# Kernel tuning notes

Hardware: AMD Instinct MI355X
Metric: run time of the kernel (lower is better)

## Reference

```python
import jax, jax.numpy as jnp
import numpy as np

N_NODES = 50000
N_EDGES = 800000
IN_CH, HID_CH, OUT_CH = 256, 128, 64


def setup_inputs() -> dict:
    key = jax.random.key(0)
    k_x, k_e, k_w1, k_w2 = jax.random.split(key, 4)
    x = jax.random.normal(k_x, (N_NODES, IN_CH), dtype=jnp.float32)
    edge_index = jax.random.randint(k_e, (2, N_EDGES), 0, N_NODES, dtype=jnp.int32)
    # Glorot-style init like PyG GCNConv (weight [in, out], bias zeros)
    s1 = float(np.sqrt(6.0 / (IN_CH + HID_CH)))
    s2 = float(np.sqrt(6.0 / (HID_CH + OUT_CH)))
    W1 = jax.random.uniform(k_w1, (IN_CH, HID_CH), jnp.float32, -s1, s1)
    b1 = jnp.zeros((HID_CH,), jnp.float32)
    W2 = jax.random.uniform(k_w2, (HID_CH, OUT_CH), jnp.float32, -s2, s2)
    b2 = jnp.zeros((OUT_CH,), jnp.float32)
    return {"x": x, "edge_index": edge_index, "W1": W1, "b1": b1, "W2": W2, "b2": b2}


def _gcn_conv(x, src, dst, deg_inv_sqrt, W, b, n_nodes):
    """GCNConv with self-loops: D^{-1/2}(A+I)D^{-1/2} X W + b."""
    h = x @ W  # [N, out]
    norm = deg_inv_sqrt[src] * deg_inv_sqrt[dst]          # [E]
    msgs = h[src] * norm[:, None]                          # [E, out] gather
    agg = jax.ops.segment_sum(msgs, dst, num_segments=n_nodes)  # scatter-add
    self_loop = h * (deg_inv_sqrt * deg_inv_sqrt)[:, None]      # self-loop term
    return agg + self_loop + b


def reference(x, edge_index, W1, b1, W2, b2):
    n = x.shape[0]
    src, dst = edge_index[0], edge_index[1]
    # degree includes self-loop (+1), edge weight 1, counted at destination
    deg = jnp.zeros((n,), x.dtype).at[dst].add(1.0) + 1.0
    dis = jax.lax.rsqrt(deg)
    h = jax.nn.relu(_gcn_conv(x, src, dst, dis, W1, b1, n))
    out = jax.nn.relu(_gcn_conv(h, src, dst, dis, W2, b2, n))
    return out
```

## Files before the change

### kernel.cpp

```cpp
#include <hip/hip_runtime.h>

#define N_NODES 50000
#define N_EDGES 800000
#define IN_CH 256
#define HID_CH 128
#define OUT_CH 64
#define CAP 64
#define NBINS 196
#define PCHUNK 3200
#define PBLOCKS 250
#define SWZ_ELEMS (IN_CH * HID_CH + HID_CH * OUT_CH)
#define SWZ_BLOCKS (SWZ_ELEMS / 256)

typedef _Float16 f16;
typedef _Float16 f16x8 __attribute__((ext_vector_type(8)));
typedef float f32x4 __attribute__((ext_vector_type(4)));
typedef unsigned short u16;
typedef unsigned int u32;

template <int K, int N>
__device__ __forceinline__ void swz(const float* __restrict__ W, f16* __restrict__ Bsw,
                                    int idx) {
    constexpr int NTILES = N / 16;
    int j = idx & 7;
    int lane = (idx >> 3) & 63;
    int rest = idx >> 9;
    int nt = rest % NTILES;
    int ks = rest / NTILES;
    int k = ks * 32 + (lane >> 4) * 8 + j;
    int n = nt * 16 + (lane & 15);
    Bsw[idx] = (f16)W[(size_t)k * N + n];
}

__device__ __forceinline__ void scan_local(const int* __restrict__ binCnt,
                                           int* sc, int* vv) {
    const int t = threadIdx.x;
    int v = (t < NBINS) ? binCnt[t] : 0;
    sc[t] = v; vv[t] = v;
    __syncthreads();
    for (int ofs = 1; ofs < 256; ofs <<= 1) {
        int add = (t >= ofs) ? sc[t - ofs] : 0;
        __syncthreads();
        sc[t] += add;
        __syncthreads();
    }
}

__global__ __launch_bounds__(256) void k_pre(const int* __restrict__ dst,
                                             int* __restrict__ binCnt,
                                             const float* __restrict__ W1,
                                             const float* __restrict__ W2,
                                             f16* __restrict__ B1,
                                             f16* __restrict__ B2) {
    if ((int)blockIdx.x < PBLOCKS) {
        __shared__ int lcnt[NBINS];
        for (int i = threadIdx.x; i < NBINS; i += 256) lcnt[i] = 0;
        __syncthreads();
        int base = blockIdx.x * PCHUNK;
        for (int i = base + (int)threadIdx.x; i < base + PCHUNK; i += 256)
            atomicAdd(&lcnt[dst[i] >> 8], 1);
        __syncthreads();
        for (int i = threadIdx.x; i < NBINS; i += 256)
            if (lcnt[i]) atomicAdd(&binCnt[i], lcnt[i]);
        return;
    }
    int idx = ((int)blockIdx.x - PBLOCKS) * 256 + threadIdx.x;
    if (idx < IN_CH * HID_CH) {
        swz<IN_CH, HID_CH>(W1, B1, idx);
    } else {
        idx -= IN_CH * HID_CH;
        if (idx < HID_CH * OUT_CH) swz<HID_CH, OUT_CH>(W2, B2, idx);
    }
}

__global__ __launch_bounds__(256) void k_place(const int* __restrict__ src,
                                               const int* __restrict__ dst,
                                               const int* __restrict__ binCnt,
                                               int* __restrict__ binCursor,
                                               u32* __restrict__ ebuf, int E) {
    __shared__ u32 codes[PCHUNK];
    __shared__ int sc[256], vv[256];
    __shared__ int lcnt[NBINS], lbase[NBINS], lcur[NBINS];
    scan_local(binCnt, sc, vv);
    for (int i = threadIdx.x; i < NBINS; i += 256) lcnt[i] = 0;
    __syncthreads();
    int base = blockIdx.x * PCHUNK;
    int m = min(PCHUNK, E - base);
    for (int j = threadIdx.x; j < m; j += 256) {
        u32 d = (u32)dst[base + j];
        codes[j] = (d << 16) | (u32)src[base + j];
        atomicAdd(&lcnt[d >> 8], 1);
    }
    __syncthreads();
    for (int i = threadIdx.x; i < NBINS; i += 256) {
        lbase[i] = (sc[i] - vv[i]) + atomicAdd(&binCursor[i], lcnt[i]);
        lcur[i] = 0;
    }
    __syncthreads();
    for (int j = threadIdx.x; j < m; j += 256) {
        u32 c = codes[j];
        int b = c >> 24;
        int p = atomicAdd(&lcur[b], 1);
        ebuf[lbase[b] + p] = c;
    }
}

__global__ __launch_bounds__(256) void k_build(const u32* __restrict__ ebuf,
                                               const int* __restrict__ binCnt,
                                               int* __restrict__ cnt,
                                               float* __restrict__ dis,
                                               u16* __restrict__ bucket, int N) {
    __shared__ int sc[256], vv[256];
    __shared__ int lcnt[256];
    __shared__ u16 lbuck[256 * CAP];
    scan_local(binCnt, sc, vv);
    int t = threadIdx.x;
    lcnt[t] = 0;
    __syncthreads();
    int b = blockIdx.x;
    int s = sc[b] - vv[b];
    int e = sc[b];
    for (int i = s + t; i < e; i += 256) {
        u32 c = ebuf[i];
        int local = (c >> 16) & 255;
        int p = atomicAdd(&lcnt[local], 1);
        if (p < CAP) lbuck[local * CAP + p] = (u16)(c & 0xFFFFu);
    }
    __syncthreads();
    int nodeBase = b << 8;
    if (nodeBase + t < N) {
        cnt[nodeBase + t] = lcnt[t];
        dis[nodeBase + t] = rsqrtf((float)lcnt[t] + 1.0f);
    }
    const uint4* lsrc = (const uint4*)lbuck;
    uint4* gdst = (uint4*)(bucket + (size_t)nodeBase * CAP);
    for (int idx = t; idx < 256 * CAP / 8; idx += 256) {
        int row = idx >> 3;
        int chunk = idx & 7;
        if (nodeBase + row < N && (chunk << 3) < lcnt[row]) gdst[idx] = lsrc[idx];
    }
}

template <int K, int N, bool A_FP32, bool RELU>
__global__ __launch_bounds__(256) void k_gemm(const void* __restrict__ Av,
                                              const f16* __restrict__ Bsw,
                                              const float* __restrict__ dis,
                                              f16* __restrict__ C, int M) {
    constexpr int KSTEPS = K / 32, NTILES = N / 16;
    const int tid = threadIdx.x;
    const int wave = tid >> 6, lane = tid & 63;
    const int quad = lane >> 4, l16 = lane & 15;
    int row = blockIdx.x * 64 + wave * 16 + l16;
    const int rowc = row < M ? row : M - 1;

    f32x4 acc[NTILES];
#pragma unroll
    for (int t = 0; t < NTILES; ++t) acc[t] = (f32x4){0.f, 0.f, 0.f, 0.f};

#pragma unroll
    for (int ks = 0; ks < KSTEPS; ++ks) {
        f16x8 afrag;
        if (A_FP32) {
            const float* A = (const float*)Av;
            const float4* p = (const float4*)(A + (size_t)rowc * K + ks * 32 + quad * 8);
            float4 v0 = p[0], v1 = p[1];
            afrag[0] = (f16)v0.x; afrag[1] = (f16)v0.y;
            afrag[2] = (f16)v0.z; afrag[3] = (f16)v0.w;
            afrag[4] = (f16)v1.x; afrag[5] = (f16)v1.y;
            afrag[6] = (f16)v1.z; afrag[7] = (f16)v1.w;
        } else {
            const f16* A = (const f16*)Av;
            afrag = *(const f16x8*)(A + (size_t)rowc * K + ks * 32 + quad * 8);
            if (RELU) {
#pragma unroll
                for (int j = 0; j < 8; ++j)
                    afrag[j] = afrag[j] > (f16)0 ? afrag[j] : (f16)0;
            }
        }
#pragma unroll
        for (int t = 0; t < NTILES; ++t) {
            f16x8 bfrag = *(const f16x8*)(Bsw + (((size_t)ks * NTILES + t) * 64 + lane) * 8);
            acc[t] = __builtin_amdgcn_mfma_f32_16x16x32_f16(afrag, bfrag, acc[t], 0, 0, 0);
        }
    }

    int rbase = blockIdx.x * 64 + wave * 16 + quad * 4;
#pragma unroll
    for (int r = 0; r < 4; ++r) {
        int gr = rbase + r;
        if (gr < M) {
            float d = dis[gr];
#pragma unroll
            for (int t = 0; t < NTILES; ++t)
                C[(size_t)gr * N + t * 16 + l16] = (f16)(acc[t][r] * d);
        }
    }
}

__global__ __launch_bounds__(256) void k_pullgemm(const f16* __restrict__ g1,
                                                  const float* __restrict__ dis,
                                                  const float* __restrict__ b1,
                                                  const int* __restrict__ cnt,
                                                  const u16* __restrict__ bucket,
                                                  const f16* __restrict__ B2sw,
                                                  f16* __restrict__ g2) {
    constexpr int LDSW = HID_CH + 8;
    __shared__ f16 aggl[64 * LDSW];
    const int tid = threadIdx.x;
    const int sub = tid & 15;
    const int nl = tid >> 4;
    const int blockBase = (int)blockIdx.x * 64;

    const float4* b1p = (const float4*)(b1 + sub * 8);
    float4 bb0 = b1p[0], bb1 = b1p[1];
    float bv[8] = {bb0.x, bb0.y, bb0.z, bb0.w, bb1.x, bb1.y, bb1.z, bb1.w};

    for (int it = 0; it < 4; ++it) {
        int lrow = it * 16 + nl;
        int u = blockBase + lrow;
        f16x8 o;
        if (u < N_NODES) {
            const f16* gp = g1 + sub * 8;
            f16x8 sv = *(const f16x8*)(gp + (size_t)u * HID_CH);
            float a[8];
#pragma unroll
            for (int j = 0; j < 8; ++j) a[j] = (float)sv[j];

            int n = cnt[u];
            if (n > CAP) n = CAP;
            const u16* row = bucket + u * CAP;

            int k = 0;
            for (; k + 8 <= n; k += 8) {
                uint4 iv = *(const uint4*)(row + k);
                int s0 = iv.x & 0xFFFF, s1 = iv.x >> 16;
                int s2 = iv.y & 0xFFFF, s3 = iv.y >> 16;
                int s4 = iv.z & 0xFFFF, s5 = iv.z >> 16;
                int s6 = iv.w & 0xFFFF, s7 = iv.w >> 16;
                f16x8 v0 = *(const f16x8*)(gp + (size_t)s0 * HID_CH);
                f16x8 v1 = *(const f16x8*)(gp + (size_t)s1 * HID_CH);
                f16x8 v2 = *(const f16x8*)(gp + (size_t)s2 * HID_CH);
                f16x8 v3 = *(const f16x8*)(gp + (size_t)s3 * HID_CH);
                f16x8 v4 = *(const f16x8*)(gp + (size_t)s4 * HID_CH);
                f16x8 v5 = *(const f16x8*)(gp + (size_t)s5 * HID_CH);
                f16x8 v6 = *(const f16x8*)(gp + (size_t)s6 * HID_CH);
                f16x8 v7 = *(const f16x8*)(gp + (size_t)s7 * HID_CH);
#pragma unroll
                for (int j = 0; j < 8; ++j)
                    a[j] += (((float)v0[j] + (float)v1[j]) + ((float)v2[j] + (float)v3[j])) +
                            (((float)v4[j] + (float)v5[j]) + ((float)v6[j] + (float)v7[j]));
            }
            if (k + 4 <= n) {
                ushort4 s4v = *(const ushort4*)(row + k);
                f16x8 v0 = *(const f16x8*)(gp + (size_t)s4v.x * HID_CH);
                f16x8 v1 = *(const f16x8*)(gp + (size_t)s4v.y * HID_CH);
                f16x8 v2 = *(const f16x8*)(gp + (size_t)s4v.z * HID_CH);
                f16x8 v3 = *(const f16x8*)(gp + (size_t)s4v.w * HID_CH);
#pragma unroll
                for (int j = 0; j < 8; ++j)
                    a[j] += ((float)v0[j] + (float)v1[j]) + ((float)v2[j] + (float)v3[j]);
                k += 4;
            }
            for (; k < n; ++k) {
                f16x8 v = *(const f16x8*)(gp + (size_t)row[k] * HID_CH);
#pragma unroll
                for (int j = 0; j < 8; ++j) a[j] += (float)v[j];
            }

            float du = dis[u];
#pragma unroll
            for (int j = 0; j < 8; ++j) {
                float t = fmaf(du, a[j], bv[j]);
                o[j] = (f16)(t > 0.f ? t : 0.f);
            }
        } else {
#pragma unroll
            for (int j = 0; j < 8; ++j) o[j] = (f16)0;
        }
        *(f16x8*)(aggl + (size_t)lrow * LDSW + sub * 8) = o;
    }
    __syncthreads();

    constexpr int KSTEPS = HID_CH / 32, NTILES = OUT_CH / 16;
    const int wave = tid >> 6, lane = tid & 63;
    const int quad = lane >> 4, l16 = lane & 15;
    const int lrowA = wave * 16 + l16;

    f32x4 acc[NTILES];
#pragma unroll
    for (int t = 0; t < NTILES; ++t) acc[t] = (f32x4){0.f, 0.f, 0.f, 0.f};

#pragma unroll
    for (int ks = 0; ks < KSTEPS; ++ks) {
        f16x8 afrag = *(const f16x8*)(aggl + (size_t)lrowA * LDSW + ks * 32 + quad * 8);
#pragma unroll
        for (int t = 0; t < NTILES; ++t) {
            f16x8 bfrag = *(const f16x8*)(B2sw + (((size_t)ks * NTILES + t) * 64 + lane) * 8);
            acc[t] = __builtin_amdgcn_mfma_f32_16x16x32_f16(afrag, bfrag, acc[t], 0, 0, 0);
        }
    }

    int rbase = blockBase + wave * 16 + quad * 4;
#pragma unroll
    for (int r = 0; r < 4; ++r) {
        int gr = rbase + r;
        if (gr < N_NODES) {
            float d = dis[gr];
#pragma unroll
            for (int t = 0; t < NTILES; ++t)
                g2[(size_t)gr * OUT_CH + t * 16 + l16] = (f16)(acc[t][r] * d);
        }
    }
}

__global__ __launch_bounds__(256) void k_pull2(const f16* __restrict__ g2,
                                               const float* __restrict__ dis,
                                               const float* __restrict__ b2,
                                               const int* __restrict__ cnt,
                                               const u16* __restrict__ bucket,
                                               float* __restrict__ out) {
    int gtid = blockIdx.x * 256 + threadIdx.x;
    int u = gtid >> 3;
    int sub = gtid & 7;
    if (u >= N_NODES) return;
    const f16* gp = g2 + sub * 8;

    f16x8 sv = *(const f16x8*)(gp + (size_t)u * OUT_CH);
    float a[8];
#pragma unroll
    for (int j = 0; j < 8; ++j) a[j] = (float)sv[j];

    int n = cnt[u];
    if (n > CAP) n = CAP;
    const u16* row = bucket + u * CAP;

    int k = 0;
    for (; k + 8 <= n; k += 8) {
        uint4 iv = *(const uint4*)(row + k);
        int s0 = iv.x & 0xFFFF, s1 = iv.x >> 16;
        int s2 = iv.y & 0xFFFF, s3 = iv.y >> 16;
        int s4 = iv.z & 0xFFFF, s5 = iv.z >> 16;
        int s6 = iv.w & 0xFFFF, s7 = iv.w >> 16;
        f16x8 v0 = *(const f16x8*)(gp + (size_t)s0 * OUT_CH);
        f16x8 v1 = *(const f16x8*)(gp + (size_t)s1 * OUT_CH);
        f16x8 v2 = *(const f16x8*)(gp + (size_t)s2 * OUT_CH);
        f16x8 v3 = *(const f16x8*)(gp + (size_t)s3 * OUT_CH);
        f16x8 v4 = *(const f16x8*)(gp + (size_t)s4 * OUT_CH);
        f16x8 v5 = *(const f16x8*)(gp + (size_t)s5 * OUT_CH);
        f16x8 v6 = *(const f16x8*)(gp + (size_t)s6 * OUT_CH);
        f16x8 v7 = *(const f16x8*)(gp + (size_t)s7 * OUT_CH);
#pragma unroll
        for (int j = 0; j < 8; ++j)
            a[j] += (((float)v0[j] + (float)v1[j]) + ((float)v2[j] + (float)v3[j])) +
                    (((float)v4[j] + (float)v5[j]) + ((float)v6[j] + (float)v7[j]));
    }
    if (k + 4 <= n) {
        ushort4 s4v = *(const ushort4*)(row + k);
        f16x8 v0 = *(const f16x8*)(gp + (size_t)s4v.x * OUT_CH);
        f16x8 v1 = *(const f16x8*)(gp + (size_t)s4v.y * OUT_CH);
        f16x8 v2 = *(const f16x8*)(gp + (size_t)s4v.z * OUT_CH);
        f16x8 v3 = *(const f16x8*)(gp + (size_t)s4v.w * OUT_CH);
#pragma unroll
        for (int j = 0; j < 8; ++j)
            a[j] += ((float)v0[j] + (float)v1[j]) + ((float)v2[j] + (float)v3[j]);
        k += 4;
    }
    for (; k < n; ++k) {
        f16x8 v = *(const f16x8*)(gp + (size_t)row[k] * OUT_CH);
#pragma unroll
        for (int j = 0; j < 8; ++j) a[j] += (float)v[j];
    }

    float du = dis[u];
    float4* op = (float4*)(out + (size_t)u * OUT_CH + sub * 8);
    float4 o0, o1;
    o0.x = fmaxf(fmaf(du, a[0], b2[sub * 8 + 0]), 0.f);
    o0.y = fmaxf(fmaf(du, a[1], b2[sub * 8 + 1]), 0.f);
    o0.z = fmaxf(fmaf(du, a[2], b2[sub * 8 + 2]), 0.f);
    o0.w = fmaxf(fmaf(du, a[3], b2[sub * 8 + 3]), 0.f);
    o1.x = fmaxf(fmaf(du, a[4], b2[sub * 8 + 4]), 0.f);
    o1.y = fmaxf(fmaf(du, a[5], b2[sub * 8 + 5]), 0.f);
    o1.z = fmaxf(fmaf(du, a[6], b2[sub * 8 + 6]), 0.f);
    o1.w = fmaxf(fmaf(du, a[7], b2[sub * 8 + 7]), 0.f);
    op[0] = o0;
    op[1] = o1;
}


extern "C" void kernel_launch(void* const* d_in, const int* in_sizes, int n_in,
                              void* d_out, int out_size, void* d_ws, size_t ws_size,
                              hipStream_t stream) {
    const float* x  = (const float*)d_in[0];
    const int* ei   = (const int*)d_in[1];
    const float* W1 = (const float*)d_in[2];
    const float* b1 = (const float*)d_in[3];
    const float* W2 = (const float*)d_in[4];
    const float* b2 = (const float*)d_in[5];
    float* out = (float*)d_out;

    const int* src = ei;
    const int* dst = ei + N_EDGES;

    char* ws = (char*)d_ws;
    size_t off = 0;
    auto alloc = [&](size_t bytes) -> void* {
        off = (off + 255) & ~(size_t)255;
        void* p = ws + off;
        off += bytes;
        return p;
    };
    int*   zbuf      = (int*)alloc((size_t)(NBINS * 2) * 4);
    int*   binCnt    = zbuf;
    int*   binCursor = zbuf + NBINS;
    u32*   ebuf      = (u32*)alloc((size_t)N_EDGES * 4);
    int*   cnt       = (int*)alloc((size_t)N_NODES * 4);
    float* dis       = (float*)alloc((size_t)N_NODES * 4);
    u16*   bucket    = (u16*)alloc((size_t)N_NODES * CAP * 2);
    f16*   W1sw      = (f16*)alloc((size_t)IN_CH * HID_CH * 2);
    f16*   W2sw      = (f16*)alloc((size_t)HID_CH * OUT_CH * 2);
    f16*   g1        = (f16*)alloc((size_t)N_NODES * HID_CH * 2);
    f16*   g2        = (f16*)alloc((size_t)N_NODES * OUT_CH * 2);

    hipMemsetAsync(zbuf, 0, (size_t)(NBINS * 2) * 4, stream);

    k_pre<<<PBLOCKS + SWZ_BLOCKS, 256, 0, stream>>>(dst, binCnt, W1, W2, W1sw, W2sw);
    k_place<<<PBLOCKS, 256, 0, stream>>>(src, dst, binCnt, binCursor, ebuf, N_EDGES);
    k_build<<<NBINS, 256, 0, stream>>>(ebuf, binCnt, cnt, dis, bucket, N_NODES);

    k_gemm<IN_CH, HID_CH, true, false><<<(N_NODES + 63) / 64, 256, 0, stream>>>(
        x, W1sw, dis, g1, N_NODES);

    k_pullgemm<<<(N_NODES + 63) / 64, 256, 0, stream>>>(g1, dis, b1, cnt, bucket,
                                                        W2sw, g2);

    k_pull2<<<(N_NODES * 8 + 255) / 256, 256, 0, stream>>>(g2, dis, b2, cnt, bucket, out);
}
```

Before: 198.5 us.

## Replace binned two-pass edge placement with direct global-atomic bucket scatter

Removes the three-kernel counting-sort pipeline (bin count, bin placement into an edge buffer, per-bin LDS bucket build) and replaces it with one kernel where each edge does a global atomicAdd on its destination's count and writes its source into a fixed-capacity per-node bucket. The degree normalisation is now computed inside the first GEMM's epilogue from cnt, so the separate dis write pass goes away. This saves two launches and the intermediate edge buffer traffic, but trades coalesced LDS-staged writes for 800K scattered global atomics and 2-byte scattered stores. Neighbour order within a bucket becomes nondeterministic, which can change floating-point summation order.

```diff
diff --git a/kernel.cpp b/kernel.cpp
--- a/kernel.cpp
+++ b/kernel.cpp
@@ -6,9 +6,7 @@
 #define HID_CH 128
 #define OUT_CH 64
 #define CAP 64
-#define NBINS 196
-#define PCHUNK 3200
-#define PBLOCKS 250
+#define SCAT_BLOCKS 3125
 #define SWZ_ELEMS (IN_CH * HID_CH + HID_CH * OUT_CH)
 #define SWZ_BLOCKS (SWZ_ELEMS / 256)
 
@@ -32,39 +30,23 @@
     Bsw[idx] = (f16)W[(size_t)k * N + n];
 }
 
-__device__ __forceinline__ void scan_local(const int* __restrict__ binCnt,
-                                           int* sc, int* vv) {
-    const int t = threadIdx.x;
-    int v = (t < NBINS) ? binCnt[t] : 0;
-    sc[t] = v; vv[t] = v;
-    __syncthreads();
-    for (int ofs = 1; ofs < 256; ofs <<= 1) {
-        int add = (t >= ofs) ? sc[t - ofs] : 0;
-        __syncthreads();
-        sc[t] += add;
-        __syncthreads();
-    }
-}
-
-__global__ __launch_bounds__(256) void k_pre(const int* __restrict__ dst,
-                                             int* __restrict__ binCnt,
-                                             const float* __restrict__ W1,
-                                             const float* __restrict__ W2,
-                                             f16* __restrict__ B1,
-                                             f16* __restrict__ B2) {
-    if ((int)blockIdx.x < PBLOCKS) {
-        __shared__ int lcnt[NBINS];
-        for (int i = threadIdx.x; i < NBINS; i += 256) lcnt[i] = 0;
-        __syncthreads();
-        int base = blockIdx.x * PCHUNK;
-        for (int i = base + (int)threadIdx.x; i < base + PCHUNK; i += 256)
-            atomicAdd(&lcnt[dst[i] >> 8], 1);
-        __syncthreads();
-        for (int i = threadIdx.x; i < NBINS; i += 256)
-            if (lcnt[i]) atomicAdd(&binCnt[i], lcnt[i]);
+__global__ __launch_bounds__(256) void k_scatter(const int* __restrict__ src,
+                                                 const int* __restrict__ dst,
+                                                 int* __restrict__ cnt,
+                                                 u16* __restrict__ bucket,
+                                                 const float* __restrict__ W1,
+                                                 const float* __restrict__ W2,
+                                                 f16* __restrict__ B1,
+                                                 f16* __restrict__ B2) {
+    if ((int)blockIdx.x < SCAT_BLOCKS) {
+        int i = (int)blockIdx.x * 256 + (int)threadIdx.x;
+        int d = dst[i];
+        int s = src[i];
+        int p = atomicAdd(&cnt[d], 1);
+        if (p < CAP) bucket[(size_t)d * CAP + p] = (u16)s;
         return;
     }
-    int idx = ((int)blockIdx.x - PBLOCKS) * 256 + threadIdx.x;
+    int idx = ((int)blockIdx.x - SCAT_BLOCKS) * 256 + threadIdx.x;
     if (idx < IN_CH * HID_CH) {
         swz<IN_CH, HID_CH>(W1, B1, idx);
     } else {
@@ -73,79 +55,12 @@
     }
 }
 
-__global__ __launch_bounds__(256) void k_place(const int* __restrict__ src,
-                                               const int* __restrict__ dst,
-                                               const int* __restrict__ binCnt,
-                                               int* __restrict__ binCursor,
-                                               u32* __restrict__ ebuf, int E) {
-    __shared__ u32 codes[PCHUNK];
-    __shared__ int sc[256], vv[256];
-    __shared__ int lcnt[NBINS], lbase[NBINS], lcur[NBINS];
-    scan_local(binCnt, sc, vv);
-    for (int i = threadIdx.x; i < NBINS; i += 256) lcnt[i] = 0;
-    __syncthreads();
-    int base = blockIdx.x * PCHUNK;
-    int m = min(PCHUNK, E - base);
-    for (int j = threadIdx.x; j < m; j += 256) {
-        u32 d = (u32)dst[base + j];
-        codes[j] = (d << 16) | (u32)src[base + j];
-        atomicAdd(&lcnt[d >> 8], 1);
-    }
-    __syncthreads();
-    for (int i = threadIdx.x; i < NBINS; i += 256) {
-        lbase[i] = (sc[i] - vv[i]) + atomicAdd(&binCursor[i], lcnt[i]);
-        lcur[i] = 0;
-    }
-    __syncthreads();
-    for (int j = threadIdx.x; j < m; j += 256) {
-        u32 c = codes[j];
-        int b = c >> 24;
-        int p = atomicAdd(&lcur[b], 1);
-        ebuf[lbase[b] + p] = c;
-    }
-}
-
-__global__ __launch_bounds__(256) void k_build(const u32* __restrict__ ebuf,
-                                               const int* __restrict__ binCnt,
-                                               int* __restrict__ cnt,
+template <int K, int N>
+__global__ __launch_bounds__(256) void k_gemm1(const float* __restrict__ A,
+                                               const f16* __restrict__ Bsw,
+                                               const int* __restrict__ cnt,
                                                float* __restrict__ dis,
-                                               u16* __restrict__ bucket, int N) {
-    __shared__ int sc[256], vv[256];
-    __shared__ int lcnt[256];
-    __shared__ u16 lbuck[256 * CAP];
-    scan_local(binCnt, sc, vv);
-    int t = threadIdx.x;
-    lcnt[t] = 0;
-    __syncthreads();
-    int b = blockIdx.x;
-    int s = sc[b] - vv[b];
-    int e = sc[b];
-    for (int i = s + t; i < e; i += 256) {
-        u32 c = ebuf[i];
-        int local = (c >> 16) & 255;
-        int p = atomicAdd(&lcnt[local], 1);
-        if (p < CAP) lbuck[local * CAP + p] = (u16)(c & 0xFFFFu);
-    }
-    __syncthreads();
-    int nodeBase = b << 8;
-    if (nodeBase + t < N) {
-        cnt[nodeBase + t] = lcnt[t];
-        dis[nodeBase + t] = rsqrtf((float)lcnt[t] + 1.0f);
-    }
-    const uint4* lsrc = (const uint4*)lbuck;
-    uint4* gdst = (uint4*)(bucket + (size_t)nodeBase * CAP);
-    for (int idx = t; idx < 256 * CAP / 8; idx += 256) {
-        int row = idx >> 3;
-        int chunk = idx & 7;
-        if (nodeBase + row < N && (chunk << 3) < lcnt[row]) gdst[idx] = lsrc[idx];
-    }
-}
-
-template <int K, int N, bool A_FP32, bool RELU>
-__global__ __launch_bounds__(256) void k_gemm(const void* __restrict__ Av,
-                                              const f16* __restrict__ Bsw,
-                                              const float* __restrict__ dis,
-                                              f16* __restrict__ C, int M) {
+                                               f16* __restrict__ C, int M) {
     constexpr int KSTEPS = K / 32, NTILES = N / 16;
     const int tid = threadIdx.x;
     const int wave = tid >> 6, lane = tid & 63;
@@ -160,23 +75,12 @@
 #pragma unroll
     for (int ks = 0; ks < KSTEPS; ++ks) {
         f16x8 afrag;
-        if (A_FP32) {
-            const float* A = (const float*)Av;
-            const float4* p = (const float4*)(A + (size_t)rowc * K + ks * 32 + quad * 8);
-            float4 v0 = p[0], v1 = p[1];
-            afrag[0] = (f16)v0.x; afrag[1] = (f16)v0.y;
-            afrag[2] = (f16)v0.z; afrag[3] = (f16)v0.w;
-            afrag[4] = (f16)v1.x; afrag[5] = (f16)v1.y;
-            afrag[6] = (f16)v1.z; afrag[7] = (f16)v1.w;
-        } else {
-            const f16* A = (const f16*)Av;
-            afrag = *(const f16x8*)(A + (size_t)rowc * K + ks * 32 + quad * 8);
-            if (RELU) {
-#pragma unroll
-                for (int j = 0; j < 8; ++j)
-                    afrag[j] = afrag[j] > (f16)0 ? afrag[j] : (f16)0;
-            }
-        }
+        const float4* p = (const float4*)(A + (size_t)rowc * K + ks * 32 + quad * 8);
+        float4 v0 = p[0], v1 = p[1];
+        afrag[0] = (f16)v0.x; afrag[1] = (f16)v0.y;
+        afrag[2] = (f16)v0.z; afrag[3] = (f16)v0.w;
+        afrag[4] = (f16)v1.x; afrag[5] = (f16)v1.y;
+        afrag[6] = (f16)v1.z; afrag[7] = (f16)v1.w;
 #pragma unroll
         for (int t = 0; t < NTILES; ++t) {
             f16x8 bfrag = *(const f16x8*)(Bsw + (((size_t)ks * NTILES + t) * 64 + lane) * 8);
@@ -189,7 +93,8 @@
     for (int r = 0; r < 4; ++r) {
         int gr = rbase + r;
         if (gr < M) {
-            float d = dis[gr];
+            float d = rsqrtf((float)cnt[gr] + 1.0f);
+            if (l16 == 0) dis[gr] = d;
 #pragma unroll
             for (int t = 0; t < NTILES; ++t)
                 C[(size_t)gr * N + t * 16 + l16] = (f16)(acc[t][r] * d);
@@ -409,10 +314,6 @@
         off += bytes;
         return p;
     };
-    int*   zbuf      = (int*)alloc((size_t)(NBINS * 2) * 4);
-    int*   binCnt    = zbuf;
-    int*   binCursor = zbuf + NBINS;
-    u32*   ebuf      = (u32*)alloc((size_t)N_EDGES * 4);
     int*   cnt       = (int*)alloc((size_t)N_NODES * 4);
     float* dis       = (float*)alloc((size_t)N_NODES * 4);
     u16*   bucket    = (u16*)alloc((size_t)N_NODES * CAP * 2);
@@ -421,14 +322,13 @@
     f16*   g1        = (f16*)alloc((size_t)N_NODES * HID_CH * 2);
     f16*   g2        = (f16*)alloc((size_t)N_NODES * OUT_CH * 2);
 
-    hipMemsetAsync(zbuf, 0, (size_t)(NBINS * 2) * 4, stream);
-
-    k_pre<<<PBLOCKS + SWZ_BLOCKS, 256, 0, stream>>>(dst, binCnt, W1, W2, W1sw, W2sw);
-    k_place<<<PBLOCKS, 256, 0, stream>>>(src, dst, binCnt, binCursor, ebuf, N_EDGES);
-    k_build<<<NBINS, 256, 0, stream>>>(ebuf, binCnt, cnt, dis, bucket, N_NODES);
-
-    k_gemm<IN_CH, HID_CH, true, false><<<(N_NODES + 63) / 64, 256, 0, stream>>>(
-        x, W1sw, dis, g1, N_NODES);
+    hipMemsetAsync(cnt, 0, (size_t)N_NODES * 4, stream);
+
+    k_scatter<<<SCAT_BLOCKS + SWZ_BLOCKS, 256, 0, stream>>>(src, dst, cnt, bucket,
+                                                            W1, W2, W1sw, W2sw);
+
+    k_gemm1<IN_CH, HID_CH><<<(N_NODES + 63) / 64, 256, 0, stream>>>(
+        x, W1sw, cnt, dis, g1, N_NODES);
 
     k_pullgemm<<<(N_NODES + 63) / 64, 256, 0, stream>>>(g1, dis, b1, cnt, bucket,
                                                         W2sw, g2);
```

Measured after the change: 206.4 us. +4.0%, slower.

## Store hidden features in column-tiled layout and stage neighbor lists in LDS

Applied to the files above, without the earlier changes.

The GEMM outputs g1 and g2 are now written in a tile-major layout, [tile][node][16], so each gather pass over one 16-column tile touches a compact 1.6 MB (g1) or smaller array that can stay in cache. The pull kernels first copy each block's neighbor index lists, counts and degree scales into shared memory, then loop over column tiles with 4 threads per node. This aims to improve L2 hit rate for the random gathers and to avoid re-reading indices from global memory. In exchange, indices are re-walked once per tile, each gather moves only 16 bytes, and the extra LDS use may lower occupancy.

```diff
diff --git a/kernel.cpp b/kernel.cpp
--- a/kernel.cpp
+++ b/kernel.cpp
@@ -6,11 +6,14 @@
 #define HID_CH 128
 #define OUT_CH 64
 #define CAP 64
+#define LBSTRIDE 72
 #define NBINS 196
 #define PCHUNK 3200
 #define PBLOCKS 250
 #define SWZ_ELEMS (IN_CH * HID_CH + HID_CH * OUT_CH)
 #define SWZ_BLOCKS (SWZ_ELEMS / 256)
+#define NT1 (HID_CH / 16)
+#define NT2 (OUT_CH / 16)
 
 typedef _Float16 f16;
 typedef _Float16 f16x8 __attribute__((ext_vector_type(8)));
@@ -141,11 +144,11 @@
     }
 }
 
-template <int K, int N, bool A_FP32, bool RELU>
-__global__ __launch_bounds__(256) void k_gemm(const void* __restrict__ Av,
-                                              const f16* __restrict__ Bsw,
-                                              const float* __restrict__ dis,
-                                              f16* __restrict__ C, int M) {
+__global__ __launch_bounds__(256) void k_gemm1(const float* __restrict__ A,
+                                               const f16* __restrict__ Bsw,
+                                               const float* __restrict__ dis,
+                                               f16* __restrict__ C, int M) {
+    constexpr int K = IN_CH, N = HID_CH;
     constexpr int KSTEPS = K / 32, NTILES = N / 16;
     const int tid = threadIdx.x;
     const int wave = tid >> 6, lane = tid & 63;
@@ -160,23 +163,12 @@
 #pragma unroll
     for (int ks = 0; ks < KSTEPS; ++ks) {
         f16x8 afrag;
-        if (A_FP32) {
-            const float* A = (const float*)Av;
-            const float4* p = (const float4*)(A + (size_t)rowc * K + ks * 32 + quad * 8);
-            float4 v0 = p[0], v1 = p[1];
-            afrag[0] = (f16)v0.x; afrag[1] = (f16)v0.y;
-            afrag[2] = (f16)v0.z; afrag[3] = (f16)v0.w;
-            afrag[4] = (f16)v1.x; afrag[5] = (f16)v1.y;
-            afrag[6] = (f16)v1.z; afrag[7] = (f16)v1.w;
-        } else {
-            const f16* A = (const f16*)Av;
-            afrag = *(const f16x8*)(A + (size_t)rowc * K + ks * 32 + quad * 8);
-            if (RELU) {
-#pragma unroll
-                for (int j = 0; j < 8; ++j)
-                    afrag[j] = afrag[j] > (f16)0 ? afrag[j] : (f16)0;
-            }
-        }
+        const float4* p = (const float4*)(A + (size_t)rowc * K + ks * 32 + quad * 8);
+        float4 v0 = p[0], v1 = p[1];
+        afrag[0] = (f16)v0.x; afrag[1] = (f16)v0.y;
+        afrag[2] = (f16)v0.z; afrag[3] = (f16)v0.w;
+        afrag[4] = (f16)v1.x; afrag[5] = (f16)v1.y;
+        afrag[6] = (f16)v1.z; afrag[7] = (f16)v1.w;
 #pragma unroll
         for (int t = 0; t < NTILES; ++t) {
             f16x8 bfrag = *(const f16x8*)(Bsw + (((size_t)ks * NTILES + t) * 64 + lane) * 8);
@@ -192,82 +184,102 @@
             float d = dis[gr];
 #pragma unroll
             for (int t = 0; t < NTILES; ++t)
-                C[(size_t)gr * N + t * 16 + l16] = (f16)(acc[t][r] * d);
-        }
-    }
-}
-
-__global__ __launch_bounds__(256) void k_pullgemm(const f16* __restrict__ g1,
+                C[((size_t)t * N_NODES + gr) * 16 + l16] = (f16)(acc[t][r] * d);
+        }
+    }
+}
+
+__global__ __launch_bounds__(256) void k_pullgemm(const f16* __restrict__ g1t,
                                                   const float* __restrict__ dis,
                                                   const float* __restrict__ b1,
                                                   const int* __restrict__ cnt,
                                                   const u16* __restrict__ bucket,
                                                   const f16* __restrict__ B2sw,
-                                                  f16* __restrict__ g2) {
+                                                  f16* __restrict__ g2t) {
     constexpr int LDSW = HID_CH + 8;
     __shared__ f16 aggl[64 * LDSW];
+    __shared__ u16 lbuck[64 * LBSTRIDE];
+    __shared__ int lcnt[64];
+    __shared__ float ldis[64];
     const int tid = threadIdx.x;
-    const int sub = tid & 15;
-    const int nl = tid >> 4;
     const int blockBase = (int)blockIdx.x * 64;
-
-    const float4* b1p = (const float4*)(b1 + sub * 8);
-    float4 bb0 = b1p[0], bb1 = b1p[1];
-    float bv[8] = {bb0.x, bb0.y, bb0.z, bb0.w, bb1.x, bb1.y, bb1.z, bb1.w};
-
-    for (int it = 0; it < 4; ++it) {
-        int lrow = it * 16 + nl;
-        int u = blockBase + lrow;
+    const int gmax = N_NODES - blockBase;
+
+    {
+        const uint4* bsrc = (const uint4*)(bucket + (size_t)blockBase * CAP);
+        for (int i = tid; i < 64 * (CAP / 8); i += 256) {
+            int r = i >> 3, c = i & 7;
+            uint4 v = make_uint4(0, 0, 0, 0);
+            if (r < gmax) v = bsrc[(r << 3) + c];
+            *(uint4*)(lbuck + r * LBSTRIDE + (c << 3)) = v;
+        }
+        if (tid < 64) {
+            int u = blockBase + tid;
+            int n = (u < N_NODES) ? cnt[u] : 0;
+            lcnt[tid] = n > CAP ? CAP : n;
+            ldis[tid] = (u < N_NODES) ? dis[u] : 0.f;
+        }
+    }
+    __syncthreads();
+
+    const int sub = tid & 1;
+    const int sl = (tid >> 1) & 1;
+    const int nl = tid >> 2;
+    const int u = blockBase + nl;
+    const int n = lcnt[nl];
+    const float du = ldis[nl];
+    const u16* lrow = lbuck + nl * LBSTRIDE;
+
+    for (int it = 0; it < NT1 / 2; ++it) {
+        int nt = it * 2 + sl;
         f16x8 o;
         if (u < N_NODES) {
-            const f16* gp = g1 + sub * 8;
-            f16x8 sv = *(const f16x8*)(gp + (size_t)u * HID_CH);
+            const f16* gp = g1t + (size_t)nt * N_NODES * 16 + sub * 8;
+            f16x8 sv = *(const f16x8*)(gp + (size_t)u * 16);
             float a[8];
 #pragma unroll
             for (int j = 0; j < 8; ++j) a[j] = (float)sv[j];
-
-            int n = cnt[u];
-            if (n > CAP) n = CAP;
-            const u16* row = bucket + u * CAP;
 
             int k = 0;
             for (; k + 8 <= n; k += 8) {
-                uint4 iv = *(const uint4*)(row + k);
+                uint4 iv = *(const uint4*)(lrow + k);
                 int s0 = iv.x & 0xFFFF, s1 = iv.x >> 16;
                 int s2 = iv.y & 0xFFFF, s3 = iv.y >> 16;
                 int s4 = iv.z & 0xFFFF, s5 = iv.z >> 16;
                 int s6 = iv.w & 0xFFFF, s7 = iv.w >> 16;
-                f16x8 v0 = *(const f16x8*)(gp + (size_t)s0 * HID_CH);
-                f16x8 v1 = *(const f16x8*)(gp + (size_t)s1 * HID_CH);
-                f16x8 v2 = *(const f16x8*)(gp + (size_t)s2 * HID_CH);
-                f16x8 v3 = *(const f16x8*)(gp + (size_t)s3 * HID_CH);
-                f16x8 v4 = *(const f16x8*)(gp + (size_t)s4 * HID_CH);
-                f16x8 v5 = *(const f16x8*)(gp + (size_t)s5 * HID_CH);
-                f16x8 v6 = *(const f16x8*)(gp + (size_t)s6 * HID_CH);
-                f16x8 v7 = *(const f16x8*)(gp + (size_t)s7 * HID_CH);
+                f16x8 v0 = *(const f16x8*)(gp + (size_t)s0 * 16);
+                f16x8 v1 = *(const f16x8*)(gp + (size_t)s1 * 16);
+                f16x8 v2 = *(const f16x8*)(gp + (size_t)s2 * 16);
+                f16x8 v3 = *(const f16x8*)(gp + (size_t)s3 * 16);
+                f16x8 v4 = *(const f16x8*)(gp + (size_t)s4 * 16);
+                f16x8 v5 = *(const f16x8*)(gp + (size_t)s5 * 16);
+                f16x8 v6 = *(const f16x8*)(gp + (size_t)s6 * 16);
+                f16x8 v7 = *(const f16x8*)(gp + (size_t)s7 * 16);
 #pragma unroll
                 for (int j = 0; j < 8; ++j)
                     a[j] += (((float)v0[j] + (float)v1[j]) + ((float)v2[j] + (float)v3[j])) +
                             (((float)v4[j] + (float)v5[j]) + ((float)v6[j] + (float)v7[j]));
             }
             if (k + 4 <= n) {
-                ushort4 s4v = *(const ushort4*)(row + k);
-                f16x8 v0 = *(const f16x8*)(gp + (size_t)s4v.x * HID_CH);
-                f16x8 v1 = *(const f16x8*)(gp + (size_t)s4v.y * HID_CH);
-                f16x8 v2 = *(const f16x8*)(gp + (size_t)s4v.z * HID_CH);
-                f16x8 v3 = *(const f16x8*)(gp + (size_t)s4v.w * HID_CH);
+                ushort4 s4v = *(const ushort4*)(lrow + k);
+                f16x8 v0 = *(const f16x8*)(gp + (size_t)s4v.x * 16);
+                f16x8 v1 = *(const f16x8*)(gp + (size_t)s4v.y * 16);
+                f16x8 v2 = *(const f16x8*)(gp + (size_t)s4v.z * 16);
+                f16x8 v3 = *(const f16x8*)(gp + (size_t)s4v.w * 16);
 #pragma unroll
                 for (int j = 0; j < 8; ++j)
                     a[j] += ((float)v0[j] + (float)v1[j]) + ((float)v2[j] + (float)v3[j]);
                 k += 4;
             }
             for (; k < n; ++k) {
-                f16x8 v = *(const f16x8*)(gp + (size_t)row[k] * HID_CH);
+                f16x8 v = *(const f16x8*)(gp + (size_t)lrow[k] * 16);
 #pragma unroll
                 for (int j = 0; j < 8; ++j) a[j] += (float)v[j];
             }
 
-            float du = dis[u];
+            const float4* bp = (const float4*)(b1 + nt * 16 + sub * 8);
+            float4 B0 = bp[0], B1v = bp[1];
+            float bv[8] = {B0.x, B0.y, B0.z, B0.w, B1v.x, B1v.y, B1v.z, B1v.w};
 #pragma unroll
             for (int j = 0; j < 8; ++j) {
                 float t = fmaf(du, a[j], bv[j]);
@@ -277,7 +289,7 @@
 #pragma unroll
             for (int j = 0; j < 8; ++j) o[j] = (f16)0;
         }
-        *(f16x8*)(aggl + (size_t)lrow * LDSW + sub * 8) = o;
+        *(f16x8*)(aggl + (size_t)nl * LDSW + nt * 16 + sub * 8) = o;
     }
     __syncthreads();
 
@@ -308,82 +320,109 @@
             float d = dis[gr];
 #pragma unroll
             for (int t = 0; t < NTILES; ++t)
-                g2[(size_t)gr * OUT_CH + t * 16 + l16] = (f16)(acc[t][r] * d);
-        }
-    }
-}
-
-__global__ __launch_bounds__(256) void k_pull2(const f16* __restrict__ g2,
+                g2t[((size_t)t * N_NODES + gr) * 16 + l16] = (f16)(acc[t][r] * d);
+        }
+    }
+}
+
+__global__ __launch_bounds__(256) void k_pull2(const f16* __restrict__ g2t,
                                                const float* __restrict__ dis,
                                                const float* __restrict__ b2,
                                                const int* __restrict__ cnt,
                                                const u16* __restrict__ bucket,
                                                float* __restrict__ out) {
-    int gtid = blockIdx.x * 256 + threadIdx.x;
-    int u = gtid >> 3;
-    int sub = gtid & 7;
+    __shared__ u16 lbuck[64 * LBSTRIDE];
+    __shared__ int lcnt[64];
+    __shared__ float ldis[64];
+    const int tid = threadIdx.x;
+    const int blockBase = (int)blockIdx.x * 64;
+    const int gmax = N_NODES - blockBase;
+
+    {
+        const uint4* bsrc = (const uint4*)(bucket + (size_t)blockBase * CAP);
+        for (int i = tid; i < 64 * (CAP / 8); i += 256) {
+            int r = i >> 3, c = i & 7;
+            uint4 v = make_uint4(0, 0, 0, 0);
+            if (r < gmax) v = bsrc[(r << 3) + c];
+            *(uint4*)(lbuck + r * LBSTRIDE + (c << 3)) = v;
+        }
+        if (tid < 64) {
+            int u = blockBase + tid;
+            int n = (u < N_NODES) ? cnt[u] : 0;
+            lcnt[tid] = n > CAP ? CAP : n;
+            ldis[tid] = (u < N_NODES) ? dis[u] : 0.f;
+        }
+    }
+    __syncthreads();
+
+    const int sub = tid & 1;
+    const int sl = (tid >> 1) & 1;
+    const int nl = tid >> 2;
+    const int u = blockBase + nl;
     if (u >= N_NODES) return;
-    const f16* gp = g2 + sub * 8;
-
-    f16x8 sv = *(const f16x8*)(gp + (size_t)u * OUT_CH);
-    float a[8];
-#pragma unroll
-    for (int j = 0; j < 8; ++j) a[j] = (float)sv[j];
-
-    int n = cnt[u];
-    if (n > CAP) n = CAP;
-    const u16* row = bucket + u * CAP;
-
-    int k = 0;
-    for (; k + 8 <= n; k += 8) {
-        uint4 iv = *(const uint4*)(row + k);
-        int s0 = iv.x & 0xFFFF, s1 = iv.x >> 16;
-        int s2 = iv.y & 0xFFFF, s3 = iv.y >> 16;
-        int s4 = iv.z & 0xFFFF, s5 = iv.z >> 16;
-        int s6 = iv.w & 0xFFFF, s7 = iv.w >> 16;
-        f16x8 v0 = *(const f16x8*)(gp + (size_t)s0 * OUT_CH);
-        f16x8 v1 = *(const f16x8*)(gp + (size_t)s1 * OUT_CH);
-        f16x8 v2 = *(const f16x8*)(gp + (size_t)s2 * OUT_CH);
-        f16x8 v3 = *(const f16x8*)(gp + (size_t)s3 * OUT_CH);
-        f16x8 v4 = *(const f16x8*)(gp + (size_t)s4 * OUT_CH);
-        f16x8 v5 = *(const f16x8*)(gp + (size_t)s5 * OUT_CH);
-        f16x8 v6 = *(const f16x8*)(gp + (size_t)s6 * OUT_CH);
-        f16x8 v7 = *(const f16x8*)(gp + (size_t)s7 * OUT_CH);
-#pragma unroll
-        for (int j = 0; j < 8; ++j)
-            a[j] += (((float)v0[j] + (float)v1[j]) + ((float)v2[j] + (float)v3[j])) +
-                    (((float)v4[j] + (float)v5[j]) + ((float)v6[j] + (float)v7[j]));
-    }
-    if (k + 4 <= n) {
-        ushort4 s4v = *(const ushort4*)(row + k);
-        f16x8 v0 = *(const f16x8*)(gp + (size_t)s4v.x * OUT_CH);
-        f16x8 v1 = *(const f16x8*)(gp + (size_t)s4v.y * OUT_CH);
-        f16x8 v2 = *(const f16x8*)(gp + (size_t)s4v.z * OUT_CH);
-        f16x8 v3 = *(const f16x8*)(gp + (size_t)s4v.w * OUT_CH);
-#pragma unroll
-        for (int j = 0; j < 8; ++j)
-            a[j] += ((float)v0[j] + (float)v1[j]) + ((float)v2[j] + (float)v3[j]);
-        k += 4;
-    }
-    for (; k < n; ++k) {
-        f16x8 v = *(const f16x8*)(gp + (size_t)row[k] * OUT_CH);
-#pragma unroll
-        for (int j = 0; j < 8; ++j) a[j] += (float)v[j];
-    }
-
-    float du = dis[u];
-    float4* op = (float4*)(out + (size_t)u * OUT_CH + sub * 8);
-    float4 o0, o1;
-    o0.x = fmaxf(fmaf(du, a[0], b2[sub * 8 + 0]), 0.f);
-    o0.y = fmaxf(fmaf(du, a[1], b2[sub * 8 + 1]), 0.f);
-    o0.z = fmaxf(fmaf(du, a[2], b2[sub * 8 + 2]), 0.f);
-    o0.w = fmaxf(fmaf(du, a[3], b2[sub * 8 + 3]), 0.f);
-    o1.x = fmaxf(fmaf(du, a[4], b2[sub * 8 + 4]), 0.f);
-    o1.y = fmaxf(fmaf(du, a[5], b2[sub * 8 + 5]), 0.f);
-    o1.z = fmaxf(fmaf(du, a[6], b2[sub * 8 + 6]), 0.f);
-    o1.w = fmaxf(fmaf(du, a[7], b2[sub * 8 + 7]), 0.f);
-    op[0] = o0;
-    op[1] = o1;
+    const int n = lcnt[nl];
+    const float du = ldis[nl];
+    const u16* lrow = lbuck + nl * LBSTRIDE;
+
+    for (int it = 0; it < NT2 / 2; ++it) {
+        int nt = it * 2 + sl;
+        const f16* gp = g2t + (size_t)nt * N_NODES * 16 + sub * 8;
+        f16x8 sv = *(const f16x8*)(gp + (size_t)u * 16);
+        float a[8];
+#pragma unroll
+        for (int j = 0; j < 8; ++j) a[j] = (float)sv[j];
+
+        int k = 0;
+        for (; k + 8 <= n; k += 8) {
+            uint4 iv = *(const uint4*)(lrow + k);
+            int s0 = iv.x & 0xFFFF, s1 = iv.x >> 16;
+            int s2 = iv.y & 0xFFFF, s3 = iv.y >> 16;
+            int s4 = iv.z & 0xFFFF, s5 = iv.z >> 16;
+            int s6 = iv.w & 0xFFFF, s7 = iv.w >> 16;
+            f16x8 v0 = *(const f16x8*)(gp + (size_t)s0 * 16);
+            f16x8 v1 = *(const f16x8*)(gp + (size_t)s1 * 16);
+            f16x8 v2 = *(const f16x8*)(gp + (size_t)s2 * 16);
+            f16x8 v3 = *(const f16x8*)(gp + (size_t)s3 * 16);
+            f16x8 v4 = *(const f16x8*)(gp + (size_t)s4 * 16);
+            f16x8 v5 = *(const f16x8*)(gp + (size_t)s5 * 16);
+            f16x8 v6 = *(const f16x8*)(gp + (size_t)s6 * 16);
+            f16x8 v7 = *(const f16x8*)(gp + (size_t)s7 * 16);
+#pragma unroll
+            for (int j = 0; j < 8; ++j)
+                a[j] += (((float)v0[j] + (float)v1[j]) + ((float)v2[j] + (float)v3[j])) +
+                        (((float)v4[j] + (float)v5[j]) + ((float)v6[j] + (float)v7[j]));
+        }
+        if (k + 4 <= n) {
+            ushort4 s4v = *(const ushort4*)(lrow + k);
+            f16x8 v0 = *(const f16x8*)(gp + (size_t)s4v.x * 16);
+            f16x8 v1 = *(const f16x8*)(gp + (size_t)s4v.y * 16);
+            f16x8 v2 = *(const f16x8*)(gp + (size_t)s4v.z * 16);
+            f16x8 v3 = *(const f16x8*)(gp + (size_t)s4v.w * 16);
+#pragma unroll
+            for (int j = 0; j < 8; ++j)
+                a[j] += ((float)v0[j] + (float)v1[j]) + ((float)v2[j] + (float)v3[j]);
+            k += 4;
+        }
+        for (; k < n; ++k) {
+            f16x8 v = *(const f16x8*)(gp + (size_t)lrow[k] * 16);
+#pragma unroll
+            for (int j = 0; j < 8; ++j) a[j] += (float)v[j];
+        }
+
+        const float* bp = b2 + nt * 16 + sub * 8;
+        float4* op = (float4*)(out + (size_t)u * OUT_CH + nt * 16 + sub * 8);
+        float4 o0, o1;
+        o0.x = fmaxf(fmaf(du, a[0], bp[0]), 0.f);
+        o0.y = fmaxf(fmaf(du, a[1], bp[1]), 0.f);
+        o0.z = fmaxf(fmaf(du, a[2], bp[2]), 0.f);
+        o0.w = fmaxf(fmaf(du, a[3], bp[3]), 0.f);
+        o1.x = fmaxf(fmaf(du, a[4], bp[4]), 0.f);
+        o1.y = fmaxf(fmaf(du, a[5], bp[5]), 0.f);
+        o1.z = fmaxf(fmaf(du, a[6], bp[6]), 0.f);
+        o1.w = fmaxf(fmaf(du, a[7], bp[7]), 0.f);
+        op[0] = o0;
+        op[1] = o1;
+    }
 }
 
 
@@ -418,8 +457,8 @@
     u16*   bucket    = (u16*)alloc((size_t)N_NODES * CAP * 2);
     f16*   W1sw      = (f16*)alloc((size_t)IN_CH * HID_CH * 2);
     f16*   W2sw      = (f16*)alloc((size_t)HID_CH * OUT_CH * 2);
-    f16*   g1        = (f16*)alloc((size_t)N_NODES * HID_CH * 2);
-    f16*   g2        = (f16*)alloc((size_t)N_NODES * OUT_CH * 2);
+    f16*   g1t       = (f16*)alloc((size_t)N_NODES * HID_CH * 2);
+    f16*   g2t       = (f16*)alloc((size_t)N_NODES * OUT_CH * 2);
 
     hipMemsetAsync(zbuf, 0, (size_t)(NBINS * 2) * 4, stream);
 
@@ -427,11 +466,10 @@
     k_place<<<PBLOCKS, 256, 0, stream>>>(src, dst, binCnt, binCursor, ebuf, N_EDGES);
     k_build<<<NBINS, 256, 0, stream>>>(ebuf, binCnt, cnt, dis, bucket, N_NODES);
 
-    k_gemm<IN_CH, HID_CH, true, false><<<(N_NODES + 63) / 64, 256, 0, stream>>>(
-        x, W1sw, dis, g1, N_NODES);
-
-    k_pullgemm<<<(N_NODES + 63) / 64, 256, 0, stream>>>(g1, dis, b1, cnt, bucket,
-                                                        W2sw, g2);
-
-    k_pull2<<<(N_NODES * 8 + 255) / 256, 256, 0, stream>>>(g2, dis, b2, cnt, bucket, out);
-}
+    k_gemm1<<<(N_NODES + 63) / 64, 256, 0, stream>>>(x, W1sw, dis, g1t, N_NODES);
+
+    k_pullgemm<<<(N_NODES + 63) / 64, 256, 0, stream>>>(g1t, dis, b1, cnt, bucket,
+                                                        W2sw, g2t);
+
+    k_pull2<<<(N_NODES + 63) / 64, 256, 0, stream>>>(g2t, dis, b2, cnt, bucket, out);
+}
```

New measurement: 224.9 us. 13.3% more time.
